# Kernel optimization log

Hardware: AMD Instinct MI355X
Metric: run time of the kernel (lower is better)

The kernel has to match this reference:

```python
import jax, jax.numpy as jnp
import numpy as np

B, T, H = 8192, 2048, 51


def _lstm_cell(x, h, c, Wih, Whh, bih, bhh):
    # PyTorch LSTMCell gate order: i, f, g, o
    gates = x @ Wih.T + bih + h @ Whh.T + bhh  # [B, 4H]
    i, f, g, o = jnp.split(gates, 4, axis=-1)
    c2 = jax.nn.sigmoid(f) * c + jax.nn.sigmoid(i) * jnp.tanh(g)
    h2 = jax.nn.sigmoid(o) * jnp.tanh(c2)
    return h2, c2


def setup_inputs() -> dict:
    key = jax.random.key(0)
    ks = jax.random.split(key, 12)
    s1 = 1.0 / np.sqrt(H)
    u = lambda k, shape: jax.random.uniform(k, shape, jnp.float32, -s1, s1)
    return {
        "x": jax.random.normal(ks[0], (B, T), dtype=jnp.float32),
        "W_ih1": u(ks[1], (4 * H, 1)),
        "W_hh1": u(ks[2], (4 * H, H)),
        "b_ih1": u(ks[3], (4 * H,)),
        "b_hh1": u(ks[4], (4 * H,)),
        "W_ih2": u(ks[5], (4 * H, H)),
        "W_hh2": u(ks[6], (4 * H, H)),
        "b_ih2": u(ks[7], (4 * H,)),
        "b_hh2": u(ks[8], (4 * H,)),
        "W_lin": u(ks[9], (1, H)),
        "b_lin": u(ks[10], (1,)),
    }


def reference(x, W_ih1, W_hh1, b_ih1, b_hh1, W_ih2, W_hh2, b_ih2, b_hh2, W_lin, b_lin):
    n = x.shape[0]
    h1 = jnp.zeros((n, H), jnp.float32)
    c1 = jnp.zeros((n, H), jnp.float32)
    h2 = jnp.zeros((n, H), jnp.float32)
    c2 = jnp.zeros((n, H), jnp.float32)

    xs = x.T[:, :, None]  # [T, B, 1]

    def step(carry, x_t):
        h1, c1, h2, c2 = carry
        h1, c1 = _lstm_cell(x_t, h1, c1, W_ih1, W_hh1, b_ih1, b_hh1)
        h2, c2 = _lstm_cell(h1, h2, c2, W_ih2, W_hh2, b_ih2, b_hh2)
        y = h2 @ W_lin.T + b_lin  # [B, 1]
        return (h1, c1, h2, c2), y

    _, ys = jax.lax.scan(step, (h1, c1, h2, c2), xs)  # ys: [T, B, 1]
    return ys[:, :, 0].T  # [B, T]
```

## Files before the change

### kernel.cpp

```cpp
#include <hip/hip_runtime.h>


#define B_TOT 8192
#define T_LEN 2048
#define MR    16
#define ROWW  72
#define HB    (MR*ROWW)

typedef _Float16 f16x8 __attribute__((ext_vector_type(8)));
typedef float    f32x4 __attribute__((ext_vector_type(4)));
typedef float    f32x2 __attribute__((ext_vector_type(2)));

#define LOG2E 1.4426950408889634f

static __device__ __forceinline__ float us2f(unsigned short u) {
    unsigned int w = ((unsigned int)u) << 16;
    float f; __builtin_memcpy(&f, &w, 4);
    return f;
}
static __device__ __forceinline__ float ldf(const void* p, int idx, bool isbf) {
    return isbf ? us2f(((const unsigned short*)p)[idx])
                : ((const float*)p)[idx];
}
static __device__ __forceinline__ void store_y(void* outp, bool isbf, int idx, float v) {
    if (isbf) {
        unsigned int u; __builtin_memcpy(&u, &v, 4);
        u = (u + 0x7FFFu + ((u >> 16) & 1u)) >> 16;
        ((unsigned short*)outp)[idx] = (unsigned short)u;
    } else {
        ((float*)outp)[idx] = v;
    }
}

template<bool CLAMP_G>
static __device__ __forceinline__ void lstm_act(const f32x4* acc, f32x2* C, f32x2* h) {
    f32x2 di[2], df[2], dg[2], dox[2];
    #pragma unroll
    for (int p = 0; p < 2; ++p) {
        f32x2 ei, ef, eg, eo;
        #pragma unroll
        for (int e = 0; e < 2; ++e) {
            const int r = 2*p + e;
            ei[e] = __builtin_amdgcn_exp2f(acc[0][r]);
            ef[e] = __builtin_amdgcn_exp2f(acc[1][r]);
            float ag = acc[2][r];
            if (CLAMP_G) ag = __builtin_amdgcn_fmed3f(ag, -30.0f, 30.0f);
            eg[e] = __builtin_amdgcn_exp2f(ag);
            eo[e] = __builtin_amdgcn_exp2f(acc[3][r]);
        }
        di[p]  = ei + 1.0f;
        df[p]  = ef + 1.0f;
        dg[p]  = eg + 1.0f;
        dox[p] = eo + 1.0f;
    }
    f32x2 q[2], sig[2];
    q[0] = di[0]*dg[0];
    q[1] = di[1]*dg[1];
    const float Ri0 = __builtin_amdgcn_rcpf(q[0].x*q[0].y);
    const float Ri1 = __builtin_amdgcn_rcpf(q[1].x*q[1].y);
    sig[0] = (dg[0]*(2.0f*LOG2E) + (-4.0f*LOG2E)) * (q[0].yx * Ri0);
    sig[1] = (dg[1]*(2.0f*LOG2E) + (-4.0f*LOG2E)) * (q[1].yx * Ri1);
    const float pf01 = df[0].x*df[0].y;
    const float pf23 = df[1].x*df[1].y;
    const float Rf   = __builtin_amdgcn_rcpf(pf01*pf23);
    const f32x2 sf0 = df[0].yx * (Rf*pf23);
    const f32x2 sf1 = df[1].yx * (Rf*pf01);
    f32x2 tt[2], m[2];
    {
        const f32x2 Cn = sf0*C[0] + sig[0];
        C[0] = Cn;
        f32x2 e2;
        e2.x = __builtin_amdgcn_exp2f(__builtin_amdgcn_fmed3f(Cn.x, -30.0f, 30.0f));
        e2.y = __builtin_amdgcn_exp2f(__builtin_amdgcn_fmed3f(Cn.y, -30.0f, 30.0f));
        tt[0] = e2 + 1.0f;
        m[0]  = dox[0]*tt[0];
    }
    {
        const f32x2 Cn = sf1*C[1] + sig[1];
        C[1] = Cn;
        f32x2 e2;
        e2.x = __builtin_amdgcn_exp2f(__builtin_amdgcn_fmed3f(Cn.x, -30.0f, 30.0f));
        e2.y = __builtin_amdgcn_exp2f(__builtin_amdgcn_fmed3f(Cn.y, -30.0f, 30.0f));
        tt[1] = e2 + 1.0f;
        m[1]  = dox[1]*tt[1];
    }
    const float Rc = __builtin_amdgcn_rcpf(m[0].x*m[0].y);
    const float Rd = __builtin_amdgcn_rcpf(m[1].x*m[1].y);
    h[0] = (2.0f - tt[0]) * (m[0].yx * Rc);
    h[1] = (2.0f - tt[1]) * (m[1].yx * Rd);
}

__global__ __launch_bounds__(512, 4)
void lstm2_kernel(const void* __restrict__ xin,
                  const void* __restrict__ Wih1, const void* __restrict__ Whh1,
                  const void* __restrict__ bih1, const void* __restrict__ bhh1,
                  const void* __restrict__ Wih2, const void* __restrict__ Whh2,
                  const void* __restrict__ bih2, const void* __restrict__ bhh2,
                  const void* __restrict__ Wlin, const void* __restrict__ blin,
                  void* __restrict__ outp)
{
    const int tid  = threadIdx.x;
    const int wset = tid >> 8;
    const int wv   = (tid >> 6) & 3;
    const int ln   = tid & 63;
    const int lid  = ln & 15;
    const int quad = ln >> 4;
    const int b0   = blockIdx.x * MR;
    const int jcol = 13*wv + lid;
    const bool valid = (lid < 13) && (jcol < 51);
    const bool ylane = (wv == 3) && (lid == 12);

    __shared__ alignas(16) _Float16 hx [2*HB];
    __shared__ alignas(16) _Float16 h2b[2*HB];

    bool isbf;
    {
        const unsigned short* xu = (const unsigned short*)xin;
        int cnt = 0;
        #pragma unroll
        for (int i = 0; i < 64; i += 2) {
            unsigned e = (xu[i] >> 7) & 0xFFu;
            cnt += (e >= 115u && e <= 131u) ? 1 : 0;
        }
        isbf = (cnt >= 16);
    }

    for (int i = tid; i < 2*HB; i += 512) {
        hx[i]  = (_Float16)0.0f;
        h2b[i] = (_Float16)0.0f;
    }
    __syncthreads();
    if (tid < MR) {
        hx[0*HB + tid*ROWW + 52] = (_Float16)1.0f;
        hx[1*HB + tid*ROWW + 52] = (_Float16)1.0f;
        hx[1*HB + tid*ROWW + 51] = (_Float16)ldf(xin, (b0 + tid)*T_LEN, isbf);
    }
    __syncthreads();

    if (wset == 0) {
        f16x8 B1[4][2];
        #pragma unroll
        for (int n = 0; n < 4; ++n) {
            const int g = 51*n + jcol;
            const float sn = (n == 2) ? -2.0f*LOG2E : -LOG2E;
            #pragma unroll
            for (int kb = 0; kb < 2; ++kb) {
                f16x8 f;
                #pragma unroll
                for (int j8 = 0; j8 < 8; ++j8) {
                    const int k = kb*32 + quad*8 + j8;
                    float v = 0.0f;
                    if (valid) {
                        if (k < 51)       v = sn * ldf(Whh1, g*51 + k, isbf);
                        else if (k == 51) v = sn * ldf(Wih1, g, isbf);
                        else if (k == 52) v = sn * (ldf(bih1, g, isbf) + ldf(bhh1, g, isbf));
                    }
                    f[j8] = (_Float16)v;
                }
                B1[n][kb] = f;
            }
        }
        f32x2 c1[2] = {{0.0f, 0.0f}, {0.0f, 0.0f}};

        #pragma unroll 2
        for (int k = 0; k <= T_LEN; ++k) {
            if (k < T_LEN) {
                const int rs = (k - 1) & 1, ws = k & 1;
                const bool xl = (tid < MR) && (k + 1 < T_LEN);
                float xnext = 0.0f;
                if (xl) xnext = ldf(xin, (b0 + tid)*T_LEN + k + 1, isbf);

                const _Float16* hp = &hx[rs*HB + lid*ROWW + quad*8];
                const f16x8 a0 = *(const f16x8*)(hp);
                const f16x8 a1 = *(const f16x8*)(hp + 32);
                f32x4 acc[4];
                __builtin_amdgcn_s_setprio(1);
                #pragma unroll
                for (int n = 0; n < 4; ++n) {
                    f32x4 z = {0.0f, 0.0f, 0.0f, 0.0f};
                    z      = __builtin_amdgcn_mfma_f32_16x16x32_f16(a0, B1[n][0], z, 0,0,0);
                    acc[n] = __builtin_amdgcn_mfma_f32_16x16x32_f16(a1, B1[n][1], z, 0,0,0);
                }
                __builtin_amdgcn_s_setprio(0);
                f32x2 h[2];
                lstm_act<false>(acc, c1, h);
                if (valid) {
                    _Float16* hw = &hx[ws*HB + (quad*4)*ROWW + jcol];
                    hw[0*ROWW] = (_Float16)h[0].x;
                    hw[1*ROWW] = (_Float16)h[0].y;
                    hw[2*ROWW] = (_Float16)h[1].x;
                    hw[3*ROWW] = (_Float16)h[1].y;
                }
                if (xl) hx[ws*HB + tid*ROWW + 51] = (_Float16)xnext;
            }
            __syncthreads();
        }
    } else {
        f16x8 B2i[4][2], B2h[4][2];
        #pragma unroll
        for (int n = 0; n < 4; ++n) {
            const int g = 51*n + jcol;
            const float sn = (n == 2) ? -2.0f*LOG2E : -LOG2E;
            #pragma unroll
            for (int kb = 0; kb < 2; ++kb) {
                f16x8 fi, fh;
                #pragma unroll
                for (int j8 = 0; j8 < 8; ++j8) {
                    const int k = kb*32 + quad*8 + j8;
                    float vi = 0.0f, vh = 0.0f;
                    if (valid) {
                        if (k < 51) {
                            vi = sn * ldf(Wih2, g*51 + k, isbf);
                            vh = sn * ldf(Whh2, g*51 + k, isbf);
                        } else if (k == 52) {
                            vi = sn * (ldf(bih2, g, isbf) + ldf(bhh2, g, isbf));
                        }
                    } else if (ylane && n == 3) {
                        if (k < 51)       vh = ldf(Wlin, k, isbf);
                        else if (k == 52) vi = ldf(blin, 0, isbf);
                    }
                    fi[j8] = (_Float16)vi; fh[j8] = (_Float16)vh;
                }
                B2i[n][kb] = fi; B2h[n][kb] = fh;
            }
        }
        const float bl = ldf(blin, 0, isbf);
        f32x2 c2[2] = {{0.0f, 0.0f}, {0.0f, 0.0f}};

        #pragma unroll 2
        for (int k = 0; k <= T_LEN; ++k) {
            if (k >= 1) {
                const int rs1 = (k - 1) & 1;
                const int rs2 = k & 1;
                const int ws2 = (k - 1) & 1;
                const _Float16* h1p = &hx [rs1*HB + lid*ROWW + quad*8];
                const _Float16* h2p = &h2b[rs2*HB + lid*ROWW + quad*8];
                const f16x8 p0 = *(const f16x8*)(h1p);
                const f16x8 p1 = *(const f16x8*)(h1p + 32);
                const f16x8 q0 = *(const f16x8*)(h2p);
                const f16x8 q1 = *(const f16x8*)(h2p + 32);
                f32x4 acc[4];
                __builtin_amdgcn_s_setprio(1);
                #pragma unroll
                for (int n = 0; n < 4; ++n) {
                    f32x4 z = {0.0f, 0.0f, 0.0f, 0.0f};
                    z      = __builtin_amdgcn_mfma_f32_16x16x32_f16(p0, B2i[n][0], z, 0,0,0);
                    z      = __builtin_amdgcn_mfma_f32_16x16x32_f16(p1, B2i[n][1], z, 0,0,0);
                    z      = __builtin_amdgcn_mfma_f32_16x16x32_f16(q0, B2h[n][0], z, 0,0,0);
                    acc[n] = __builtin_amdgcn_mfma_f32_16x16x32_f16(q1, B2h[n][1], z, 0,0,0);
                }
                __builtin_amdgcn_s_setprio(0);
                if (ylane && k >= 2) {
                    #pragma unroll
                    for (int r = 0; r < 4; ++r)
                        store_y(outp, isbf, (b0 + quad*4 + r)*T_LEN + (k - 2), acc[3][r]);
                }
                f32x2 h[2];
                lstm_act<true>(acc, c2, h);
                if (valid) {
                    _Float16* hw = &h2b[ws2*HB + (quad*4)*ROWW + jcol];
                    hw[0*ROWW] = (_Float16)h[0].x;
                    hw[1*ROWW] = (_Float16)h[0].y;
                    hw[2*ROWW] = (_Float16)h[1].x;
                    hw[3*ROWW] = (_Float16)h[1].y;
                }
            }
            __syncthreads();
        }

        if (wv == 3) {
            const _Float16* h2p = &h2b[((T_LEN - 1) & 1)*HB + lid*ROWW + quad*8];
            const f16x8 q0 = *(const f16x8*)(h2p);
            const f16x8 q1 = *(const f16x8*)(h2p + 32);
            f32x4 z = {bl, bl, bl, bl};
            z = __builtin_amdgcn_mfma_f32_16x16x32_f16(q0, B2h[3][0], z, 0,0,0);
            z = __builtin_amdgcn_mfma_f32_16x16x32_f16(q1, B2h[3][1], z, 0,0,0);
            if (lid == 12) {
                #pragma unroll
                for (int r = 0; r < 4; ++r)
                    store_y(outp, isbf, (b0 + quad*4 + r)*T_LEN + (T_LEN - 1), z[r]);
            }
        }
    }
}

extern "C" void kernel_launch(void* const* d_in, const int* in_sizes, int n_in,
                              void* d_out, int out_size, void* d_ws, size_t ws_size,
                              hipStream_t stream) {
    (void)in_sizes; (void)n_in; (void)out_size; (void)d_ws; (void)ws_size;
    dim3 grid(B_TOT / MR), block(512);
    lstm2_kernel<<<grid, block, 0, stream>>>(
        d_in[0], d_in[1], d_in[2], d_in[3], d_in[4], d_in[5],
        d_in[6], d_in[7], d_in[8], d_in[9], d_in[10], d_out);
}
```

Measured before the change: 2.319 ms.

## Single-buffer LSTM hidden state with two barriers per step and split layer-2 MFMAs

Replaces the double-buffered shared-memory hidden states with single buffers and uses two barriers per timestep to separate reads from writes. Layer 2's input-projection MFMAs on h1 are issued before its own activation and h2 write, and the recurrent MFMAs on h2 run after the second barrier. Accumulators alternate between two register sets so the activation of step k-1 overlaps the h1 MFMAs of step k. The aim is to shorten the per-step critical path and shrink LDS, at the cost of an extra barrier per step and a deeper pipeline skew.

```diff
diff --git a/kernel.cpp b/kernel.cpp
--- a/kernel.cpp
+++ b/kernel.cpp
@@ -6,6 +6,7 @@
 #define MR    16
 #define ROWW  72
 #define HB    (MR*ROWW)
+#define KITER 2052
 
 typedef _Float16 f16x8 __attribute__((ext_vector_type(8)));
 typedef float    f32x4 __attribute__((ext_vector_type(4)));
@@ -110,8 +111,8 @@
     const bool valid = (lid < 13) && (jcol < 51);
     const bool ylane = (wv == 3) && (lid == 12);
 
-    __shared__ alignas(16) _Float16 hx [2*HB];
-    __shared__ alignas(16) _Float16 h2b[2*HB];
+    __shared__ alignas(16) _Float16 hx [HB];
+    __shared__ alignas(16) _Float16 h2b[HB];
 
     bool isbf;
     {
@@ -125,17 +126,15 @@
         isbf = (cnt >= 16);
     }
 
-    for (int i = tid; i < 2*HB; i += 512) {
+    for (int i = tid; i < HB; i += 512) {
         hx[i]  = (_Float16)0.0f;
         h2b[i] = (_Float16)0.0f;
     }
     __syncthreads();
     if (tid < MR) {
-        hx[0*HB + tid*ROWW + 52] = (_Float16)1.0f;
-        hx[1*HB + tid*ROWW + 52] = (_Float16)1.0f;
-        hx[1*HB + tid*ROWW + 51] = (_Float16)ldf(xin, (b0 + tid)*T_LEN, isbf);
-    }
-    __syncthreads();
+        hx[tid*ROWW + 52] = (_Float16)1.0f;
+        hx[tid*ROWW + 51] = (_Float16)ldf(xin, (b0 + tid)*T_LEN, isbf);
+    }
 
     if (wset == 0) {
         f16x8 B1[4][2];
@@ -161,39 +160,40 @@
             }
         }
         f32x2 c1[2] = {{0.0f, 0.0f}, {0.0f, 0.0f}};
-
-        #pragma unroll 2
-        for (int k = 0; k <= T_LEN; ++k) {
-            if (k < T_LEN) {
-                const int rs = (k - 1) & 1, ws = k & 1;
-                const bool xl = (tid < MR) && (k + 1 < T_LEN);
-                float xnext = 0.0f;
+        f32x4 acc1[4];
+
+        for (int k = 0; k < KITER; ++k) {
+            __syncthreads();
+            const bool run = (k < T_LEN);
+            const bool xl  = run && (tid < MR) && (k + 1 < T_LEN);
+            float xnext = 0.0f;
+            if (run) {
                 if (xl) xnext = ldf(xin, (b0 + tid)*T_LEN + k + 1, isbf);
-
-                const _Float16* hp = &hx[rs*HB + lid*ROWW + quad*8];
+                const _Float16* hp = &hx[lid*ROWW + quad*8];
                 const f16x8 a0 = *(const f16x8*)(hp);
                 const f16x8 a1 = *(const f16x8*)(hp + 32);
-                f32x4 acc[4];
                 __builtin_amdgcn_s_setprio(1);
                 #pragma unroll
                 for (int n = 0; n < 4; ++n) {
                     f32x4 z = {0.0f, 0.0f, 0.0f, 0.0f};
-                    z      = __builtin_amdgcn_mfma_f32_16x16x32_f16(a0, B1[n][0], z, 0,0,0);
-                    acc[n] = __builtin_amdgcn_mfma_f32_16x16x32_f16(a1, B1[n][1], z, 0,0,0);
+                    z       = __builtin_amdgcn_mfma_f32_16x16x32_f16(a0, B1[n][0], z, 0,0,0);
+                    acc1[n] = __builtin_amdgcn_mfma_f32_16x16x32_f16(a1, B1[n][1], z, 0,0,0);
                 }
                 __builtin_amdgcn_s_setprio(0);
+            }
+            __syncthreads();
+            if (run) {
                 f32x2 h[2];
-                lstm_act<false>(acc, c1, h);
+                lstm_act<false>(acc1, c1, h);
                 if (valid) {
-                    _Float16* hw = &hx[ws*HB + (quad*4)*ROWW + jcol];
+                    _Float16* hw = &hx[(quad*4)*ROWW + jcol];
                     hw[0*ROWW] = (_Float16)h[0].x;
                     hw[1*ROWW] = (_Float16)h[0].y;
                     hw[2*ROWW] = (_Float16)h[1].x;
                     hw[3*ROWW] = (_Float16)h[1].y;
                 }
-                if (xl) hx[ws*HB + tid*ROWW + 51] = (_Float16)xnext;
-            }
-            __syncthreads();
+                if (xl) hx[tid*ROWW + 51] = (_Float16)xnext;
+            }
         }
     } else {
         f16x8 B2i[4][2], B2h[4][2];
@@ -224,63 +224,62 @@
                 B2i[n][kb] = fi; B2h[n][kb] = fh;
             }
         }
-        const float bl = ldf(blin, 0, isbf);
         f32x2 c2[2] = {{0.0f, 0.0f}, {0.0f, 0.0f}};
-
-        #pragma unroll 2
-        for (int k = 0; k <= T_LEN; ++k) {
-            if (k >= 1) {
-                const int rs1 = (k - 1) & 1;
-                const int rs2 = k & 1;
-                const int ws2 = (k - 1) & 1;
-                const _Float16* h1p = &hx [rs1*HB + lid*ROWW + quad*8];
-                const _Float16* h2p = &h2b[rs2*HB + lid*ROWW + quad*8];
-                const f16x8 p0 = *(const f16x8*)(h1p);
-                const f16x8 p1 = *(const f16x8*)(h1p + 32);
-                const f16x8 q0 = *(const f16x8*)(h2p);
-                const f16x8 q1 = *(const f16x8*)(h2p + 32);
-                f32x4 acc[4];
-                __builtin_amdgcn_s_setprio(1);
-                #pragma unroll
-                for (int n = 0; n < 4; ++n) {
-                    f32x4 z = {0.0f, 0.0f, 0.0f, 0.0f};
-                    z      = __builtin_amdgcn_mfma_f32_16x16x32_f16(p0, B2i[n][0], z, 0,0,0);
-                    z      = __builtin_amdgcn_mfma_f32_16x16x32_f16(p1, B2i[n][1], z, 0,0,0);
-                    z      = __builtin_amdgcn_mfma_f32_16x16x32_f16(q0, B2h[n][0], z, 0,0,0);
-                    acc[n] = __builtin_amdgcn_mfma_f32_16x16x32_f16(q1, B2h[n][1], z, 0,0,0);
-                }
-                __builtin_amdgcn_s_setprio(0);
-                if (ylane && k >= 2) {
-                    #pragma unroll
-                    for (int r = 0; r < 4; ++r)
-                        store_y(outp, isbf, (b0 + quad*4 + r)*T_LEN + (k - 2), acc[3][r]);
-                }
-                f32x2 h[2];
-                lstm_act<true>(acc, c2, h);
-                if (valid) {
-                    _Float16* hw = &h2b[ws2*HB + (quad*4)*ROWW + jcol];
-                    hw[0*ROWW] = (_Float16)h[0].x;
-                    hw[1*ROWW] = (_Float16)h[0].y;
-                    hw[2*ROWW] = (_Float16)h[1].x;
-                    hw[3*ROWW] = (_Float16)h[1].y;
-                }
-            }
-            __syncthreads();
-        }
-
-        if (wv == 3) {
-            const _Float16* h2p = &h2b[((T_LEN - 1) & 1)*HB + lid*ROWW + quad*8];
-            const f16x8 q0 = *(const f16x8*)(h2p);
-            const f16x8 q1 = *(const f16x8*)(h2p + 32);
-            f32x4 z = {bl, bl, bl, bl};
-            z = __builtin_amdgcn_mfma_f32_16x16x32_f16(q0, B2h[3][0], z, 0,0,0);
-            z = __builtin_amdgcn_mfma_f32_16x16x32_f16(q1, B2h[3][1], z, 0,0,0);
-            if (lid == 12) {
-                #pragma unroll
-                for (int r = 0; r < 4; ++r)
-                    store_y(outp, isbf, (b0 + quad*4 + r)*T_LEN + (T_LEN - 1), z[r]);
-            }
-        }
+        f32x4 accP[4], accQ[4];
+
+        #define L2STEP(KV, AN, AO) do {                                          \
+            const int k_ = (KV);                                                 \
+            __syncthreads();                                           \
+            const bool mf_ = (k_ >= 1) && (k_ <= T_LEN + 1);                     \
+            if (mf_) {                      \
+                const _Float16* h1p_ = &hx[lid*ROWW + quad*8];                   \
+                const f16x8 p0_ = *(const f16x8*)(h1p_);                         \
+                const f16x8 p1_ = *(const f16x8*)(h1p_ + 32);                    \
+                __builtin_amdgcn_s_setprio(1);                                   \
+                _Pragma("unroll")                                                \
+                for (int n = 0; n < 4; ++n) {                                    \
+                    f32x4 z_ = {0.0f, 0.0f, 0.0f, 0.0f};                         \
+                    z_    = __builtin_amdgcn_mfma_f32_16x16x32_f16(p0_, B2i[n][0], z_, 0,0,0); \
+                    AN[n] = __builtin_amdgcn_mfma_f32_16x16x32_f16(p1_, B2i[n][1], z_, 0,0,0); \
+                }                                                                \
+                __builtin_amdgcn_s_setprio(0);                                   \
+            }                                                                    \
+            if (ylane && k_ >= 3 && k_ <= T_LEN + 2) {       \
+                _Pragma("unroll")                                                \
+                for (int r = 0; r < 4; ++r)                                      \
+                    store_y(outp, isbf, (b0 + quad*4 + r)*T_LEN + (k_ - 3), AO[3][r]); \
+            }                                                                    \
+            if (k_ >= 2 && k_ <= T_LEN + 1) {    \
+                f32x2 hh_[2];                                                    \
+                lstm_act<true>(AO, c2, hh_);        \
+                if (valid) {                                                     \
+                    _Float16* hw_ = &h2b[(quad*4)*ROWW + jcol];                  \
+                    hw_[0*ROWW] = (_Float16)hh_[0].x;                            \
+                    hw_[1*ROWW] = (_Float16)hh_[0].y;                            \
+                    hw_[2*ROWW] = (_Float16)hh_[1].x;                            \
+                    hw_[3*ROWW] = (_Float16)hh_[1].y;                            \
+                }                                                                \
+            }                                                                    \
+            __syncthreads();                                           \
+            if (mf_) {         \
+                const _Float16* h2p_ = &h2b[lid*ROWW + quad*8];                  \
+                const f16x8 q0_ = *(const f16x8*)(h2p_);                         \
+                const f16x8 q1_ = *(const f16x8*)(h2p_ + 32);                    \
+                __builtin_amdgcn_s_setprio(1);                                   \
+                _Pragma("unroll")                                                \
+                for (int n = 0; n < 4; ++n) {                                    \
+                    AN[n] = __builtin_amdgcn_mfma_f32_16x16x32_f16(q0_, B2h[n][0], AN[n], 0,0,0); \
+                    AN[n] = __builtin_amdgcn_mfma_f32_16x16x32_f16(q1_, B2h[n][1], AN[n], 0,0,0); \
+                }                                                                \
+                __builtin_amdgcn_s_setprio(0);                                   \
+            }                                                                    \
+        } while (0)
+
+        for (int kp = 0; kp < KITER/2; ++kp) {
+            L2STEP(2*kp,     accP, accQ);
+            L2STEP(2*kp + 1, accQ, accP);
+        }
+        #undef L2STEP
     }
 }
 
```

After: 2.800 ms. 20.7% more time.

## Process two 16-row batch tiles per block to interleave independent LSTM recurrences

Applied to the files above, without the earlier changes.

Doubles the rows handled per block from 16 to 32 and halves the grid. Each wave now issues MFMAs and activations for two independent 16-row tiles per timestep, in both layer-1 and layer-2 loops. The same weight fragments in registers serve both tiles. This is meant to hide MFMA and activation latency and to spread barrier cost over more work. The trade-off is that fewer blocks are launched, which can leave CUs with lower occupancy. It also roughly doubles LDS use and raises register pressure.

```diff
diff --git a/kernel.cpp b/kernel.cpp
--- a/kernel.cpp
+++ b/kernel.cpp
@@ -3,9 +3,10 @@
 
 #define B_TOT 8192
 #define T_LEN 2048
-#define MR    16
+#define MR    32
 #define ROWW  72
 #define HB    (MR*ROWW)
+#define T1    (16*ROWW)
 
 typedef _Float16 f16x8 __attribute__((ext_vector_type(8)));
 typedef float    f32x4 __attribute__((ext_vector_type(4)));
@@ -160,7 +161,8 @@
                 B1[n][kb] = f;
             }
         }
-        f32x2 c1[2] = {{0.0f, 0.0f}, {0.0f, 0.0f}};
+        f32x2 c1a[2] = {{0.0f, 0.0f}, {0.0f, 0.0f}};
+        f32x2 c1b[2] = {{0.0f, 0.0f}, {0.0f, 0.0f}};
 
         #pragma unroll 2
         for (int k = 0; k <= T_LEN; ++k) {
@@ -170,26 +172,42 @@
                 float xnext = 0.0f;
                 if (xl) xnext = ldf(xin, (b0 + tid)*T_LEN + k + 1, isbf);
 
-                const _Float16* hp = &hx[rs*HB + lid*ROWW + quad*8];
-                const f16x8 a0 = *(const f16x8*)(hp);
-                const f16x8 a1 = *(const f16x8*)(hp + 32);
-                f32x4 acc[4];
+                const _Float16* hpa = &hx[rs*HB + lid*ROWW + quad*8];
+                const f16x8 a0 = *(const f16x8*)(hpa);
+                const f16x8 a1 = *(const f16x8*)(hpa + 32);
+                const f16x8 b0f = *(const f16x8*)(hpa + T1);
+                const f16x8 b1f = *(const f16x8*)(hpa + T1 + 32);
+                f32x4 accA[4], accB[4];
                 __builtin_amdgcn_s_setprio(1);
                 #pragma unroll
                 for (int n = 0; n < 4; ++n) {
                     f32x4 z = {0.0f, 0.0f, 0.0f, 0.0f};
-                    z      = __builtin_amdgcn_mfma_f32_16x16x32_f16(a0, B1[n][0], z, 0,0,0);
-                    acc[n] = __builtin_amdgcn_mfma_f32_16x16x32_f16(a1, B1[n][1], z, 0,0,0);
+                    z       = __builtin_amdgcn_mfma_f32_16x16x32_f16(a0, B1[n][0], z, 0,0,0);
+                    accA[n] = __builtin_amdgcn_mfma_f32_16x16x32_f16(a1, B1[n][1], z, 0,0,0);
+                }
+                #pragma unroll
+                for (int n = 0; n < 4; ++n) {
+                    f32x4 z = {0.0f, 0.0f, 0.0f, 0.0f};
+                    z       = __builtin_amdgcn_mfma_f32_16x16x32_f16(b0f, B1[n][0], z, 0,0,0);
+                    accB[n] = __builtin_amdgcn_mfma_f32_16x16x32_f16(b1f, B1[n][1], z, 0,0,0);
                 }
                 __builtin_amdgcn_s_setprio(0);
-                f32x2 h[2];
-                lstm_act<false>(acc, c1, h);
+                f32x2 ha[2], hb[2];
+                lstm_act<false>(accA, c1a, ha);
                 if (valid) {
                     _Float16* hw = &hx[ws*HB + (quad*4)*ROWW + jcol];
-                    hw[0*ROWW] = (_Float16)h[0].x;
-                    hw[1*ROWW] = (_Float16)h[0].y;
-                    hw[2*ROWW] = (_Float16)h[1].x;
-                    hw[3*ROWW] = (_Float16)h[1].y;
+                    hw[0*ROWW] = (_Float16)ha[0].x;
+                    hw[1*ROWW] = (_Float16)ha[0].y;
+                    hw[2*ROWW] = (_Float16)ha[1].x;
+                    hw[3*ROWW] = (_Float16)ha[1].y;
+                }
+                lstm_act<false>(accB, c1b, hb);
+                if (valid) {
+                    _Float16* hw = &hx[ws*HB + T1 + (quad*4)*ROWW + jcol];
+                    hw[0*ROWW] = (_Float16)hb[0].x;
+                    hw[1*ROWW] = (_Float16)hb[0].y;
+                    hw[2*ROWW] = (_Float16)hb[1].x;
+                    hw[3*ROWW] = (_Float16)hb[1].y;
                 }
                 if (xl) hx[ws*HB + tid*ROWW + 51] = (_Float16)xnext;
             }
@@ -225,7 +243,8 @@
             }
         }
         const float bl = ldf(blin, 0, isbf);
-        f32x2 c2[2] = {{0.0f, 0.0f}, {0.0f, 0.0f}};
+        f32x2 c2a[2] = {{0.0f, 0.0f}, {0.0f, 0.0f}};
+        f32x2 c2b[2] = {{0.0f, 0.0f}, {0.0f, 0.0f}};
 
         #pragma unroll 2
         for (int k = 0; k <= T_LEN; ++k) {
@@ -239,30 +258,52 @@
                 const f16x8 p1 = *(const f16x8*)(h1p + 32);
                 const f16x8 q0 = *(const f16x8*)(h2p);
                 const f16x8 q1 = *(const f16x8*)(h2p + 32);
-                f32x4 acc[4];
+                const f16x8 p0b = *(const f16x8*)(h1p + T1);
+                const f16x8 p1b = *(const f16x8*)(h1p + T1 + 32);
+                const f16x8 q0b = *(const f16x8*)(h2p + T1);
+                const f16x8 q1b = *(const f16x8*)(h2p + T1 + 32);
+                f32x4 accA[4], accB[4];
                 __builtin_amdgcn_s_setprio(1);
                 #pragma unroll
                 for (int n = 0; n < 4; ++n) {
                     f32x4 z = {0.0f, 0.0f, 0.0f, 0.0f};
-                    z      = __builtin_amdgcn_mfma_f32_16x16x32_f16(p0, B2i[n][0], z, 0,0,0);
-                    z      = __builtin_amdgcn_mfma_f32_16x16x32_f16(p1, B2i[n][1], z, 0,0,0);
-                    z      = __builtin_amdgcn_mfma_f32_16x16x32_f16(q0, B2h[n][0], z, 0,0,0);
-                    acc[n] = __builtin_amdgcn_mfma_f32_16x16x32_f16(q1, B2h[n][1], z, 0,0,0);
+                    z       = __builtin_amdgcn_mfma_f32_16x16x32_f16(p0, B2i[n][0], z, 0,0,0);
+                    z       = __builtin_amdgcn_mfma_f32_16x16x32_f16(p1, B2i[n][1], z, 0,0,0);
+                    z       = __builtin_amdgcn_mfma_f32_16x16x32_f16(q0, B2h[n][0], z, 0,0,0);
+                    accA[n] = __builtin_amdgcn_mfma_f32_16x16x32_f16(q1, B2h[n][1], z, 0,0,0);
+                }
+                #pragma unroll
+                for (int n = 0; n < 4; ++n) {
+                    f32x4 z = {0.0f, 0.0f, 0.0f, 0.0f};
+                    z       = __builtin_amdgcn_mfma_f32_16x16x32_f16(p0b, B2i[n][0], z, 0,0,0);
+                    z       = __builtin_amdgcn_mfma_f32_16x16x32_f16(p1b, B2i[n][1], z, 0,0,0);
+                    z       = __builtin_amdgcn_mfma_f32_16x16x32_f16(q0b, B2h[n][0], z, 0,0,0);
+                    accB[n] = __builtin_amdgcn_mfma_f32_16x16x32_f16(q1b, B2h[n][1], z, 0,0,0);
                 }
                 __builtin_amdgcn_s_setprio(0);
                 if (ylane && k >= 2) {
                     #pragma unroll
-                    for (int r = 0; r < 4; ++r)
-                        store_y(outp, isbf, (b0 + quad*4 + r)*T_LEN + (k - 2), acc[3][r]);
-                }
-                f32x2 h[2];
-                lstm_act<true>(acc, c2, h);
+                    for (int r = 0; r < 4; ++r) {
+                        store_y(outp, isbf, (b0 + quad*4 + r)*T_LEN + (k - 2), accA[3][r]);
+                        store_y(outp, isbf, (b0 + 16 + quad*4 + r)*T_LEN + (k - 2), accB[3][r]);
+                    }
+                }
+                f32x2 ha[2], hb[2];
+                lstm_act<true>(accA, c2a, ha);
                 if (valid) {
                     _Float16* hw = &h2b[ws2*HB + (quad*4)*ROWW + jcol];
-                    hw[0*ROWW] = (_Float16)h[0].x;
-                    hw[1*ROWW] = (_Float16)h[0].y;
-                    hw[2*ROWW] = (_Float16)h[1].x;
-                    hw[3*ROWW] = (_Float16)h[1].y;
+                    hw[0*ROWW] = (_Float16)ha[0].x;
+                    hw[1*ROWW] = (_Float16)ha[0].y;
+                    hw[2*ROWW] = (_Float16)ha[1].x;
+                    hw[3*ROWW] = (_Float16)ha[1].y;
+                }
+                lstm_act<true>(accB, c2b, hb);
+                if (valid) {
+                    _Float16* hw = &h2b[ws2*HB + T1 + (quad*4)*ROWW + jcol];
+                    hw[0*ROWW] = (_Float16)hb[0].x;
+                    hw[1*ROWW] = (_Float16)hb[0].y;
+                    hw[2*ROWW] = (_Float16)hb[1].x;
+                    hw[3*ROWW] = (_Float16)hb[1].y;
                 }
             }
             __syncthreads();
@@ -272,13 +313,20 @@
             const _Float16* h2p = &h2b[((T_LEN - 1) & 1)*HB + lid*ROWW + quad*8];
             const f16x8 q0 = *(const f16x8*)(h2p);
             const f16x8 q1 = *(const f16x8*)(h2p + 32);
-            f32x4 z = {bl, bl, bl, bl};
-            z = __builtin_amdgcn_mfma_f32_16x16x32_f16(q0, B2h[3][0], z, 0,0,0);
-            z = __builtin_amdgcn_mfma_f32_16x16x32_f16(q1, B2h[3][1], z, 0,0,0);
+            const f16x8 q0b = *(const f16x8*)(h2p + T1);
+            const f16x8 q1b = *(const f16x8*)(h2p + T1 + 32);
+            f32x4 za = {bl, bl, bl, bl};
+            za = __builtin_amdgcn_mfma_f32_16x16x32_f16(q0, B2h[3][0], za, 0,0,0);
+            za = __builtin_amdgcn_mfma_f32_16x16x32_f16(q1, B2h[3][1], za, 0,0,0);
+            f32x4 zb = {bl, bl, bl, bl};
+            zb = __builtin_amdgcn_mfma_f32_16x16x32_f16(q0b, B2h[3][0], zb, 0,0,0);
+            zb = __builtin_amdgcn_mfma_f32_16x16x32_f16(q1b, B2h[3][1], zb, 0,0,0);
             if (lid == 12) {
                 #pragma unroll
-                for (int r = 0; r < 4; ++r)
-                    store_y(outp, isbf, (b0 + quad*4 + r)*T_LEN + (T_LEN - 1), z[r]);
+                for (int r = 0; r < 4; ++r) {
+                    store_y(outp, isbf, (b0 + quad*4 + r)*T_LEN + (T_LEN - 1), za[r]);
+                    store_y(outp, isbf, (b0 + 16 + quad*4 + r)*T_LEN + (T_LEN - 1), zb[r]);
+                }
             }
         }
     }
```

After: 7.868 ms. 3.39x slower.

## Merge warp-specialized layer wave sets into single waves computing both LSTM layers

Applied to the files above, without the earlier changes.

The kernel drops the split where one 256-thread wave set ran layer 1 and another ran layer 2 and the output projection. Blocks now have 256 threads, and each wave holds the weight fragments for both layers. Each wave issues the layer-1 and layer-2 MFMAs and both activations every step, with the loop extended by one step to emit the final output. This halves the threads taking part in each block barrier and lets the two layers' independent MFMA chains interleave within a wave. The cost is a longer serial dependency chain per wave, more VGPRs for weights, and fewer resident waves to hide latency.

```diff
diff --git a/kernel.cpp b/kernel.cpp
--- a/kernel.cpp
+++ b/kernel.cpp
@@ -90,7 +90,7 @@
     h[1] = (2.0f - tt[1]) * (m[1].yx * Rd);
 }
 
-__global__ __launch_bounds__(512, 4)
+__global__ __launch_bounds__(256, 2)
 void lstm2_kernel(const void* __restrict__ xin,
                   const void* __restrict__ Wih1, const void* __restrict__ Whh1,
                   const void* __restrict__ bih1, const void* __restrict__ bhh1,
@@ -100,8 +100,7 @@
                   void* __restrict__ outp)
 {
     const int tid  = threadIdx.x;
-    const int wset = tid >> 8;
-    const int wv   = (tid >> 6) & 3;
+    const int wv   = tid >> 6;
     const int ln   = tid & 63;
     const int lid  = ln & 15;
     const int quad = ln >> 4;
@@ -125,7 +124,7 @@
         isbf = (cnt >= 16);
     }
 
-    for (int i = tid; i < 2*HB; i += 512) {
+    for (int i = tid; i < 2*HB; i += 256) {
         hx[i]  = (_Float16)0.0f;
         h2b[i] = (_Float16)0.0f;
     }
@@ -137,150 +136,110 @@
     }
     __syncthreads();
 
-    if (wset == 0) {
-        f16x8 B1[4][2];
+    f16x8 B1[4][2], B2i[4][2], B2h[4][2];
+    #pragma unroll
+    for (int n = 0; n < 4; ++n) {
+        const int g = 51*n + jcol;
+        const float sn = (n == 2) ? -2.0f*LOG2E : -LOG2E;
         #pragma unroll
-        for (int n = 0; n < 4; ++n) {
-            const int g = 51*n + jcol;
-            const float sn = (n == 2) ? -2.0f*LOG2E : -LOG2E;
-            #pragma unroll
-            for (int kb = 0; kb < 2; ++kb) {
-                f16x8 f;
-                #pragma unroll
-                for (int j8 = 0; j8 < 8; ++j8) {
-                    const int k = kb*32 + quad*8 + j8;
-                    float v = 0.0f;
-                    if (valid) {
-                        if (k < 51)       v = sn * ldf(Whh1, g*51 + k, isbf);
-                        else if (k == 51) v = sn * ldf(Wih1, g, isbf);
-                        else if (k == 52) v = sn * (ldf(bih1, g, isbf) + ldf(bhh1, g, isbf));
+        for (int kb = 0; kb < 2; ++kb) {
+            f16x8 f1, fi, fh;
+            #pragma unroll
+            for (int j8 = 0; j8 < 8; ++j8) {
+                const int k = kb*32 + quad*8 + j8;
+                float v1 = 0.0f, vi = 0.0f, vh = 0.0f;
+                if (valid) {
+                    if (k < 51) {
+                        v1 = sn * ldf(Whh1, g*51 + k, isbf);
+                        vi = sn * ldf(Wih2, g*51 + k, isbf);
+                        vh = sn * ldf(Whh2, g*51 + k, isbf);
+                    } else if (k == 51) {
+                        v1 = sn * ldf(Wih1, g, isbf);
+                    } else if (k == 52) {
+                        v1 = sn * (ldf(bih1, g, isbf) + ldf(bhh1, g, isbf));
+                        vi = sn * (ldf(bih2, g, isbf) + ldf(bhh2, g, isbf));
                     }
-                    f[j8] = (_Float16)v;
+                } else if (ylane && n == 3) {
+                    if (k < 51)       vh = ldf(Wlin, k, isbf);
+                    else if (k == 52) vi = ldf(blin, 0, isbf);
                 }
-                B1[n][kb] = f;
-            }
-        }
-        f32x2 c1[2] = {{0.0f, 0.0f}, {0.0f, 0.0f}};
-
-        #pragma unroll 2
-        for (int k = 0; k <= T_LEN; ++k) {
-            if (k < T_LEN) {
-                const int rs = (k - 1) & 1, ws = k & 1;
-                const bool xl = (tid < MR) && (k + 1 < T_LEN);
-                float xnext = 0.0f;
-                if (xl) xnext = ldf(xin, (b0 + tid)*T_LEN + k + 1, isbf);
-
-                const _Float16* hp = &hx[rs*HB + lid*ROWW + quad*8];
-                const f16x8 a0 = *(const f16x8*)(hp);
-                const f16x8 a1 = *(const f16x8*)(hp + 32);
-                f32x4 acc[4];
-                __builtin_amdgcn_s_setprio(1);
-                #pragma unroll
-                for (int n = 0; n < 4; ++n) {
-                    f32x4 z = {0.0f, 0.0f, 0.0f, 0.0f};
-                    z      = __builtin_amdgcn_mfma_f32_16x16x32_f16(a0, B1[n][0], z, 0,0,0);
-                    acc[n] = __builtin_amdgcn_mfma_f32_16x16x32_f16(a1, B1[n][1], z, 0,0,0);
-                }
-                __builtin_amdgcn_s_setprio(0);
-                f32x2 h[2];
-                lstm_act<false>(acc, c1, h);
-                if (valid) {
-                    _Float16* hw = &hx[ws*HB + (quad*4)*ROWW + jcol];
-                    hw[0*ROWW] = (_Float16)h[0].x;
-                    hw[1*ROWW] = (_Float16)h[0].y;
-                    hw[2*ROWW] = (_Float16)h[1].x;
-                    hw[3*ROWW] = (_Float16)h[1].y;
-                }
-                if (xl) hx[ws*HB + tid*ROWW + 51] = (_Float16)xnext;
-            }
-            __syncthreads();
-        }
-    } else {
-        f16x8 B2i[4][2], B2h[4][2];
-        #pragma unroll
-        for (int n = 0; n < 4; ++n) {
-            const int g = 51*n + jcol;
-            const float sn = (n == 2) ? -2.0f*LOG2E : -LOG2E;
-            #pragma unroll
-            for (int kb = 0; kb < 2; ++kb) {
-                f16x8 fi, fh;
-                #pragma unroll
-                for (int j8 = 0; j8 < 8; ++j8) {
-                    const int k = kb*32 + quad*8 + j8;
-                    float vi = 0.0f, vh = 0.0f;
-                    if (valid) {
-                        if (k < 51) {
-                            vi = sn * ldf(Wih2, g*51 + k, isbf);
-                            vh = sn * ldf(Whh2, g*51 + k, isbf);
-                        } else if (k == 52) {
-                            vi = sn * (ldf(bih2, g, isbf) + ldf(bhh2, g, isbf));
-                        }
-                    } else if (ylane && n == 3) {
-                        if (k < 51)       vh = ldf(Wlin, k, isbf);
-                        else if (k == 52) vi = ldf(blin, 0, isbf);
-                    }
-                    fi[j8] = (_Float16)vi; fh[j8] = (_Float16)vh;
-                }
-                B2i[n][kb] = fi; B2h[n][kb] = fh;
-            }
-        }
-        const float bl = ldf(blin, 0, isbf);
-        f32x2 c2[2] = {{0.0f, 0.0f}, {0.0f, 0.0f}};
-
-        #pragma unroll 2
-        for (int k = 0; k <= T_LEN; ++k) {
-            if (k >= 1) {
-                const int rs1 = (k - 1) & 1;
-                const int rs2 = k & 1;
-                const int ws2 = (k - 1) & 1;
-                const _Float16* h1p = &hx [rs1*HB + lid*ROWW + quad*8];
-                const _Float16* h2p = &h2b[rs2*HB + lid*ROWW + quad*8];
-                const f16x8 p0 = *(const f16x8*)(h1p);
-                const f16x8 p1 = *(const f16x8*)(h1p + 32);
-                const f16x8 q0 = *(const f16x8*)(h2p);
-                const f16x8 q1 = *(const f16x8*)(h2p + 32);
-                f32x4 acc[4];
-                __builtin_amdgcn_s_setprio(1);
-                #pragma unroll
-                for (int n = 0; n < 4; ++n) {
-                    f32x4 z = {0.0f, 0.0f, 0.0f, 0.0f};
-                    z      = __builtin_amdgcn_mfma_f32_16x16x32_f16(p0, B2i[n][0], z, 0,0,0);
-                    z      = __builtin_amdgcn_mfma_f32_16x16x32_f16(p1, B2i[n][1], z, 0,0,0);
-                    z      = __builtin_amdgcn_mfma_f32_16x16x32_f16(q0, B2h[n][0], z, 0,0,0);
-                    acc[n] = __builtin_amdgcn_mfma_f32_16x16x32_f16(q1, B2h[n][1], z, 0,0,0);
-                }
-                __builtin_amdgcn_s_setprio(0);
-                if (ylane && k >= 2) {
-                    #pragma unroll
-                    for (int r = 0; r < 4; ++r)
-                        store_y(outp, isbf, (b0 + quad*4 + r)*T_LEN + (k - 2), acc[3][r]);
-                }
-                f32x2 h[2];
-                lstm_act<true>(acc, c2, h);
-                if (valid) {
-                    _Float16* hw = &h2b[ws2*HB + (quad*4)*ROWW + jcol];
-                    hw[0*ROWW] = (_Float16)h[0].x;
-                    hw[1*ROWW] = (_Float16)h[0].y;
-                    hw[2*ROWW] = (_Float16)h[1].x;
-                    hw[3*ROWW] = (_Float16)h[1].y;
-                }
-            }
-            __syncthreads();
-        }
-
-        if (wv == 3) {
-            const _Float16* h2p = &h2b[((T_LEN - 1) & 1)*HB + lid*ROWW + quad*8];
-            const f16x8 q0 = *(const f16x8*)(h2p);
-            const f16x8 q1 = *(const f16x8*)(h2p + 32);
-            f32x4 z = {bl, bl, bl, bl};
-            z = __builtin_amdgcn_mfma_f32_16x16x32_f16(q0, B2h[3][0], z, 0,0,0);
-            z = __builtin_amdgcn_mfma_f32_16x16x32_f16(q1, B2h[3][1], z, 0,0,0);
-            if (lid == 12) {
-                #pragma unroll
-                for (int r = 0; r < 4; ++r)
-                    store_y(outp, isbf, (b0 + quad*4 + r)*T_LEN + (T_LEN - 1), z[r]);
-            }
-        }
+                f1[j8] = (_Float16)v1; fi[j8] = (_Float16)vi; fh[j8] = (_Float16)vh;
+            }
+            B1[n][kb] = f1; B2i[n][kb] = fi; B2h[n][kb] = fh;
+        }
+    }
+    f32x2 c1[2] = {{0.0f, 0.0f}, {0.0f, 0.0f}};
+    f32x2 c2[2] = {{0.0f, 0.0f}, {0.0f, 0.0f}};
+
+    #pragma unroll 2
+    for (int k = 0; k <= T_LEN + 1; ++k) {
+        const int rs1 = (k - 1) & 1, ws1 = k & 1;
+        const int rs2 = k & 1,       ws2 = (k - 1) & 1;
+        const bool run1 = (k < T_LEN);
+        const bool mf2  = (k >= 1);
+        const bool act2on = (k >= 1) && (k <= T_LEN);
+        const bool xl = run1 && (tid < MR) && (k + 1 < T_LEN);
+        float xnext = 0.0f;
+        if (xl) xnext = ldf(xin, (b0 + tid)*T_LEN + k + 1, isbf);
+
+        const _Float16* h1p = &hx [rs1*HB + lid*ROWW + quad*8];
+        const _Float16* h2p = &h2b[rs2*HB + lid*ROWW + quad*8];
+        const f16x8 a0 = *(const f16x8*)(h1p);
+        const f16x8 a1 = *(const f16x8*)(h1p + 32);
+        const f16x8 q0 = *(const f16x8*)(h2p);
+        const f16x8 q1 = *(const f16x8*)(h2p + 32);
+
+        f32x4 acc1[4], acc2[4];
+        __builtin_amdgcn_s_setprio(1);
+        if (run1) {
+            #pragma unroll
+            for (int n = 0; n < 4; ++n) {
+                f32x4 z = {0.0f, 0.0f, 0.0f, 0.0f};
+                z       = __builtin_amdgcn_mfma_f32_16x16x32_f16(a0, B1[n][0], z, 0,0,0);
+                acc1[n] = __builtin_amdgcn_mfma_f32_16x16x32_f16(a1, B1[n][1], z, 0,0,0);
+            }
+        }
+        if (mf2) {
+            #pragma unroll
+            for (int n = 0; n < 4; ++n) {
+                f32x4 z = {0.0f, 0.0f, 0.0f, 0.0f};
+                z       = __builtin_amdgcn_mfma_f32_16x16x32_f16(a0, B2i[n][0], z, 0,0,0);
+                z       = __builtin_amdgcn_mfma_f32_16x16x32_f16(a1, B2i[n][1], z, 0,0,0);
+                z       = __builtin_amdgcn_mfma_f32_16x16x32_f16(q0, B2h[n][0], z, 0,0,0);
+                acc2[n] = __builtin_amdgcn_mfma_f32_16x16x32_f16(q1, B2h[n][1], z, 0,0,0);
+            }
+        }
+        __builtin_amdgcn_s_setprio(0);
+
+        if (run1) {
+            f32x2 h1o[2];
+            lstm_act<false>(acc1, c1, h1o);
+            if (valid) {
+                _Float16* hw = &hx[ws1*HB + (quad*4)*ROWW + jcol];
+                hw[0*ROWW] = (_Float16)h1o[0].x;
+                hw[1*ROWW] = (_Float16)h1o[0].y;
+                hw[2*ROWW] = (_Float16)h1o[1].x;
+                hw[3*ROWW] = (_Float16)h1o[1].y;
+            }
+            if (xl) hx[ws1*HB + tid*ROWW + 51] = (_Float16)xnext;
+        }
+        if (ylane && k >= 2) {
+            #pragma unroll
+            for (int r = 0; r < 4; ++r)
+                store_y(outp, isbf, (b0 + quad*4 + r)*T_LEN + (k - 2), acc2[3][r]);
+        }
+        if (act2on) {
+            f32x2 h2o[2];
+            lstm_act<true>(acc2, c2, h2o);
+            if (valid) {
+                _Float16* hw = &h2b[ws2*HB + (quad*4)*ROWW + jcol];
+                hw[0*ROWW] = (_Float16)h2o[0].x;
+                hw[1*ROWW] = (_Float16)h2o[0].y;
+                hw[2*ROWW] = (_Float16)h2o[1].x;
+                hw[3*ROWW] = (_Float16)h2o[1].y;
+            }
+        }
+        __syncthreads();
     }
 }
 
@@ -288,7 +247,7 @@
                               void* d_out, int out_size, void* d_ws, size_t ws_size,
                               hipStream_t stream) {
     (void)in_sizes; (void)n_in; (void)out_size; (void)d_ws; (void)ws_size;
-    dim3 grid(B_TOT / MR), block(512);
+    dim3 grid(B_TOT / MR), block(256);
     lstm2_kernel<<<grid, block, 0, stream>>>(
         d_in[0], d_in[1], d_in[2], d_in[3], d_in[4], d_in[5],
         d_in[6], d_in[7], d_in[8], d_in[9], d_in[10], d_out);
```

Result: slower. 2.776 ms (+19.7%).
